# Kernel tuning notes

Measured on AMD Instinct MI355X. Metric: run time of the kernel, lower is better.

## Reference

```python
import jax, jax.numpy as jnp
import numpy as np

N_NODES = 100000
N_EDGES = 1600000
D_IN = 128
D_OUT = 128
DROP_P = 0.5


def setup_inputs() -> dict:
    key = jax.random.key(0)
    k1, k2, k3, k4, k5, k6 = jax.random.split(key, 6)
    x = jax.random.normal(k1, (N_NODES, D_IN), dtype=jnp.float32)
    # xavier_normal init for w
    std = (2.0 / (D_IN + D_OUT)) ** 0.5
    w = jax.random.normal(k2, (D_IN, D_OUT), dtype=jnp.float32) * std
    b = jax.random.normal(k3, (D_OUT,), dtype=jnp.float32) * 0.01
    edge_row = jax.random.randint(k4, (N_EDGES,), 0, N_NODES, dtype=jnp.int32)
    edge_col = jax.random.randint(k5, (N_EDGES,), 0, N_NODES, dtype=jnp.int32)
    # normalized adjacency weights (e.g. 1/sqrt(d_i d_j)); use uniform positives
    edge_val = jax.random.uniform(k6, (N_EDGES,), dtype=jnp.float32)
    # dropout mask: keep with prob (1-p), scaled by 1/(1-p)
    km = jax.random.fold_in(key, 7)
    keep = jax.random.uniform(km, (N_NODES, D_IN)) >= DROP_P
    dropout_mask = keep.astype(jnp.float32) / (1.0 - DROP_P)
    return {"x": x, "w": w, "b": b, "edge_row": edge_row,
            "edge_col": edge_col, "edge_val": edge_val,
            "dropout_mask": dropout_mask}


def reference(x, w, b, edge_row, edge_col, edge_val, dropout_mask):
    # dropout (training mode) -> dense mm -> spmm(adj, xw) -> +b -> relu
    h = (x * dropout_mask) @ w                      # [N, D_OUT]
    msgs = h[edge_col] * edge_val[:, None]          # gather src feats, scale [E, D_OUT]
    agg = jax.ops.segment_sum(msgs, edge_row, num_segments=N_NODES)  # scatter-add to dst
    return jax.nn.relu(agg + b)
```

## Files before the change

kernel.cpp:

```cpp
#include <hip/hip_runtime.h>

#define N_NODES 100000
#define N_EDGES 1600000
#define D 128
#define MAXDEG 48

#define GEMM_NB ((N_NODES + 63) / 64)
#define HIST_NB (N_EDGES / 256)
#define TOTAL_NB (GEMM_NB + HIST_NB)

typedef __attribute__((ext_vector_type(8))) short short8;
typedef __attribute__((ext_vector_type(4))) short short4v;
typedef __attribute__((ext_vector_type(4))) float floatx4;

__device__ __forceinline__ short f2bf(float f) {
    unsigned u = __float_as_uint(f);
    u += 0x7FFFu + ((u >> 16) & 1u);
    return (short)(u >> 16);
}

#define LDSK 136
__global__ __launch_bounds__(256) void gemm_hist_fill(const float* __restrict__ x,
                                                      const float* __restrict__ mask,
                                                      const float* __restrict__ w,
                                                      unsigned short* __restrict__ h,
                                                      const int* __restrict__ erow,
                                                      const int* __restrict__ ecol,
                                                      const float* __restrict__ eval,
                                                      int* __restrict__ deg,
                                                      unsigned long long* __restrict__ pairs) {
    const unsigned bid = blockIdx.x;
    if (bid % 5 != 0 || bid >= 5 * GEMM_NB) {
        const int hist_idx = (int)(bid - bid / 5 - 1 + (bid >= 5u * GEMM_NB ? 1u : 0u))
                           - (bid >= 5u * GEMM_NB ? (int)(bid - 5u * GEMM_NB) - (int)(bid - 5u * GEMM_NB) : 0);
        const int hi = (bid < 5u * GEMM_NB) ? (int)(bid - bid / 5 - 1) : (int)(bid - GEMM_NB);
        const int e = hi * 256 + threadIdx.x;
        const int r = erow[e];
        const int k = atomicAdd(&deg[r], 1);
        if (k < MAXDEG) {
            const unsigned long long v =
                (unsigned long long)(unsigned)ecol[e] |
                ((unsigned long long)(unsigned)__float_as_uint(eval[e]) << 32);
            __builtin_nontemporal_store(v, pairs + (size_t)r * MAXDEG + k);
        }
        return;
    }
    const int gb = (int)(bid / 5);

    __shared__ short w_s[128 * LDSK];
    const int t = threadIdx.x;

#pragma unroll
    for (int i = 0; i < 4; ++i) {
        const int id = t + 256 * i;
        const int n0 = (id & 31) * 4;
        const int k0 = (id >> 5) * 4;
        short tr[4][4];
#pragma unroll
        for (int r = 0; r < 4; ++r) {
            const float4 wv = *(const float4*)(w + (size_t)(k0 + r) * D + n0);
            tr[r][0] = f2bf(wv.x); tr[r][1] = f2bf(wv.y);
            tr[r][2] = f2bf(wv.z); tr[r][3] = f2bf(wv.w);
        }
#pragma unroll
        for (int c = 0; c < 4; ++c) {
            short4v v = {tr[0][c], tr[1][c], tr[2][c], tr[3][c]};
            *(short4v*)(&w_s[(n0 + c) * LDSK + k0]) = v;
        }
    }
    __syncthreads();

    const int wave = t >> 6, lane = t & 63;
    const int m = lane & 15, quad = lane >> 4;
    const int r0w = gb * 64 + wave * 16;
    int arow = r0w + m;
    if (arow >= N_NODES) arow = N_NODES - 1;
    const float* xp = x + (size_t)arow * D;
    const float* mp = mask + (size_t)arow * D;

    floatx4 acc[8];
#pragma unroll
    for (int tt = 0; tt < 8; ++tt) acc[tt] = (floatx4){0.f, 0.f, 0.f, 0.f};

#pragma unroll
    for (int kc = 0; kc < 4; ++kc) {
        const int kb = kc * 32 + quad * 8;
        const float4 xa = *(const float4*)(xp + kb);
        const float4 xb = *(const float4*)(xp + kb + 4);
        const float4 ma = *(const float4*)(mp + kb);
        const float4 mb = *(const float4*)(mp + kb + 4);
        short8 a;
        a[0] = f2bf(xa.x * ma.x); a[1] = f2bf(xa.y * ma.y);
        a[2] = f2bf(xa.z * ma.z); a[3] = f2bf(xa.w * ma.w);
        a[4] = f2bf(xb.x * mb.x); a[5] = f2bf(xb.y * mb.y);
        a[6] = f2bf(xb.z * mb.z); a[7] = f2bf(xb.w * mb.w);
#pragma unroll
        for (int tt = 0; tt < 8; ++tt) {
            const short8 bfrag = *(const short8*)(&w_s[(tt * 16 + m) * LDSK + kb]);
            acc[tt] = __builtin_amdgcn_mfma_f32_16x16x32_bf16(a, bfrag, acc[tt], 0, 0, 0);
        }
    }

    __syncthreads();
    short* ep = w_s + wave * 16 * LDSK;
#pragma unroll
    for (int tt = 0; tt < 8; ++tt) {
        const int col = tt * 16 + m;
#pragma unroll
        for (int i = 0; i < 4; ++i)
            ep[(quad * 4 + i) * LDSK + col] = f2bf(acc[tt][i]);
    }
    __syncthreads();

    const int rrow = lane >> 2;
    const int chunk = lane & 3;
    const int gr = r0w + rrow;
    if (gr < N_NODES) {
        const short* src = ep + rrow * LDSK + chunk * 32;
        unsigned short* dst = h + (size_t)gr * D + chunk * 32;
#pragma unroll
        for (int j = 0; j < 4; ++j)
            *(short8*)(dst + j * 8) = *(const short8*)(src + j * 8);
    }
}

__global__ __launch_bounds__(256) void gather_kernel(const unsigned* __restrict__ h2,
                                                     const int* __restrict__ deg,
                                                     const int2* __restrict__ pairs,
                                                     const float* __restrict__ b,
                                                     float* __restrict__ out) {
    const int row = blockIdx.x * 4 + (threadIdx.x >> 6);
    const int lane = threadIdx.x & 63;

    int dg = deg[row];
    if (dg > MAXDEG) dg = MAXDEG;
    int p = row * MAXDEG;
    const int end = p + dg;

    float accx = 0.f, accy = 0.f;
    for (; p + 7 < end; p += 8) {
        int2 pr[8];
        unsigned u[8];
#pragma unroll
        for (int j = 0; j < 8; ++j) pr[j] = pairs[p + j];
#pragma unroll
        for (int j = 0; j < 8; ++j) u[j] = h2[(size_t)pr[j].x * 64 + lane];
#pragma unroll
        for (int j = 0; j < 8; ++j) {
            const float v = __int_as_float(pr[j].y);
            accx += __uint_as_float(u[j] << 16) * v;
            accy += __uint_as_float(u[j] & 0xFFFF0000u) * v;
        }
    }
    for (; p < end; ++p) {
        const int2 p0 = pairs[p];
        const unsigned u0 = h2[(size_t)p0.x * 64 + lane];
        const float v0 = __int_as_float(p0.y);
        accx += __uint_as_float(u0 << 16) * v0;
        accy += __uint_as_float(u0 & 0xFFFF0000u) * v0;
    }

    const float2 bv = ((const float2*)b)[lane];
    float2 o;
    o.x = fmaxf(accx + bv.x, 0.f);
    o.y = fmaxf(accy + bv.y, 0.f);
    ((float2*)(out + (size_t)row * D))[lane] = o;
}

extern "C" void kernel_launch(void* const* d_in, const int* in_sizes, int n_in,
                              void* d_out, int out_size, void* d_ws, size_t ws_size,
                              hipStream_t stream) {
    const float* x    = (const float*)d_in[0];
    const float* w    = (const float*)d_in[1];
    const float* b    = (const float*)d_in[2];
    const int*   erow = (const int*)d_in[3];
    const int*   ecol = (const int*)d_in[4];
    const float* eval = (const float*)d_in[5];
    const float* mask = (const float*)d_in[6];
    float* out = (float*)d_out;

    char* base = (char*)d_ws;
    unsigned short* h = (unsigned short*)(base);
    int* deg          = (int*)(base + 25600000);
    unsigned long long* pairs = (unsigned long long*)(base + 26000000);

    hipMemsetAsync(deg, 0, N_NODES * sizeof(int), stream);

    gemm_hist_fill<<<TOTAL_NB, 256, 0, stream>>>(x, mask, w, h, erow, ecol, eval, deg, pairs);
    gather_kernel<<<N_NODES / 4, 256, 0, stream>>>((const unsigned*)h, deg,
                                                   (const int2*)pairs, b, out);
}
```

Baseline: 339.1 us.

## Split fused GEMM/histogram kernel and add nontemporal loads and stores

Separates the interleaved GEMM and edge-bucketing blocks into two kernels, hist_fill and gemm_mfma, that run back-to-back on the same stream. It also switches streaming accesses (edge arrays, x, mask, pairs, output) to nontemporal loads and stores so they pollute the cache less. This removes the block-index decoding and branch divergence of the fused kernel. In exchange it adds a launch and loses the overlap between the atomic-heavy histogram and the compute-bound GEMM.

After: 383.1 us. 13.0% more time.

```diff
diff --git a/kernel.cpp b/kernel.cpp
--- a/kernel.cpp
+++ b/kernel.cpp
@@ -6,12 +6,11 @@
 #define MAXDEG 48
 
 #define GEMM_NB ((N_NODES + 63) / 64)
-#define HIST_NB (N_EDGES / 256)
-#define TOTAL_NB (GEMM_NB + HIST_NB)
 
 typedef __attribute__((ext_vector_type(8))) short short8;
 typedef __attribute__((ext_vector_type(4))) short short4v;
 typedef __attribute__((ext_vector_type(4))) float floatx4;
+typedef __attribute__((ext_vector_type(2))) float floatx2;
 
 __device__ __forceinline__ short f2bf(float f) {
     unsigned u = __float_as_uint(f);
@@ -19,34 +18,29 @@
     return (short)(u >> 16);
 }
 
+__global__ __launch_bounds__(256) void hist_fill(const int* __restrict__ erow,
+                                                 const int* __restrict__ ecol,
+                                                 const float* __restrict__ eval,
+                                                 int* __restrict__ deg,
+                                                 unsigned long long* __restrict__ pairs) {
+    const int e = blockIdx.x * 256 + threadIdx.x;
+    const int r = __builtin_nontemporal_load(erow + e);
+    const int k = atomicAdd(&deg[r], 1);
+    const int c = __builtin_nontemporal_load(ecol + e);
+    const float v = __builtin_nontemporal_load(eval + e);
+    if (k < MAXDEG) {
+        const unsigned long long pv =
+            (unsigned long long)(unsigned)c |
+            ((unsigned long long)(unsigned)__float_as_uint(v) << 32);
+        __builtin_nontemporal_store(pv, pairs + (size_t)r * MAXDEG + k);
+    }
+}
+
 #define LDSK 136
-__global__ __launch_bounds__(256) void gemm_hist_fill(const float* __restrict__ x,
-                                                      const float* __restrict__ mask,
-                                                      const float* __restrict__ w,
-                                                      unsigned short* __restrict__ h,
-                                                      const int* __restrict__ erow,
-                                                      const int* __restrict__ ecol,
-                                                      const float* __restrict__ eval,
-                                                      int* __restrict__ deg,
-                                                      unsigned long long* __restrict__ pairs) {
-    const unsigned bid = blockIdx.x;
-    if (bid % 5 != 0 || bid >= 5 * GEMM_NB) {
-        const int hist_idx = (int)(bid - bid / 5 - 1 + (bid >= 5u * GEMM_NB ? 1u : 0u))
-                           - (bid >= 5u * GEMM_NB ? (int)(bid - 5u * GEMM_NB) - (int)(bid - 5u * GEMM_NB) : 0);
-        const int hi = (bid < 5u * GEMM_NB) ? (int)(bid - bid / 5 - 1) : (int)(bid - GEMM_NB);
-        const int e = hi * 256 + threadIdx.x;
-        const int r = erow[e];
-        const int k = atomicAdd(&deg[r], 1);
-        if (k < MAXDEG) {
-            const unsigned long long v =
-                (unsigned long long)(unsigned)ecol[e] |
-                ((unsigned long long)(unsigned)__float_as_uint(eval[e]) << 32);
-            __builtin_nontemporal_store(v, pairs + (size_t)r * MAXDEG + k);
-        }
-        return;
-    }
-    const int gb = (int)(bid / 5);
-
+__global__ __launch_bounds__(256) void gemm_mfma(const float* __restrict__ x,
+                                                 const float* __restrict__ mask,
+                                                 const float* __restrict__ w,
+                                                 unsigned short* __restrict__ h) {
     __shared__ short w_s[128 * LDSK];
     const int t = threadIdx.x;
 
@@ -72,11 +66,11 @@
 
     const int wave = t >> 6, lane = t & 63;
     const int m = lane & 15, quad = lane >> 4;
-    const int r0w = gb * 64 + wave * 16;
+    const int r0w = blockIdx.x * 64 + wave * 16;
     int arow = r0w + m;
     if (arow >= N_NODES) arow = N_NODES - 1;
-    const float* xp = x + (size_t)arow * D;
-    const float* mp = mask + (size_t)arow * D;
+    const floatx4* xp4 = (const floatx4*)(x + (size_t)arow * D);
+    const floatx4* mp4 = (const floatx4*)(mask + (size_t)arow * D);
 
     floatx4 acc[8];
 #pragma unroll
@@ -85,15 +79,15 @@
 #pragma unroll
     for (int kc = 0; kc < 4; ++kc) {
         const int kb = kc * 32 + quad * 8;
-        const float4 xa = *(const float4*)(xp + kb);
-        const float4 xb = *(const float4*)(xp + kb + 4);
-        const float4 ma = *(const float4*)(mp + kb);
-        const float4 mb = *(const float4*)(mp + kb + 4);
+        const floatx4 xa = __builtin_nontemporal_load(xp4 + kb / 4);
+        const floatx4 xb = __builtin_nontemporal_load(xp4 + kb / 4 + 1);
+        const floatx4 ma = __builtin_nontemporal_load(mp4 + kb / 4);
+        const floatx4 mb = __builtin_nontemporal_load(mp4 + kb / 4 + 1);
         short8 a;
-        a[0] = f2bf(xa.x * ma.x); a[1] = f2bf(xa.y * ma.y);
-        a[2] = f2bf(xa.z * ma.z); a[3] = f2bf(xa.w * ma.w);
-        a[4] = f2bf(xb.x * mb.x); a[5] = f2bf(xb.y * mb.y);
-        a[6] = f2bf(xb.z * mb.z); a[7] = f2bf(xb.w * mb.w);
+#pragma unroll
+        for (int j = 0; j < 4; ++j) a[j] = f2bf(xa[j] * ma[j]);
+#pragma unroll
+        for (int j = 0; j < 4; ++j) a[4 + j] = f2bf(xb[j] * mb[j]);
 #pragma unroll
         for (int tt = 0; tt < 8; ++tt) {
             const short8 bfrag = *(const short8*)(&w_s[(tt * 16 + m) * LDSK + kb]);
@@ -126,7 +120,7 @@
 
 __global__ __launch_bounds__(256) void gather_kernel(const unsigned* __restrict__ h2,
                                                      const int* __restrict__ deg,
-                                                     const int2* __restrict__ pairs,
+                                                     const unsigned long long* __restrict__ pairs,
                                                      const float* __restrict__ b,
                                                      float* __restrict__ out) {
     const int row = blockIdx.x * 4 + (threadIdx.x >> 6);
@@ -139,32 +133,32 @@
 
     float accx = 0.f, accy = 0.f;
     for (; p + 7 < end; p += 8) {
-        int2 pr[8];
+        unsigned long long pr[8];
         unsigned u[8];
 #pragma unroll
-        for (int j = 0; j < 8; ++j) pr[j] = pairs[p + j];
+        for (int j = 0; j < 8; ++j) pr[j] = __builtin_nontemporal_load(pairs + p + j);
 #pragma unroll
-        for (int j = 0; j < 8; ++j) u[j] = h2[(size_t)pr[j].x * 64 + lane];
+        for (int j = 0; j < 8; ++j) u[j] = h2[(size_t)(unsigned)(pr[j] & 0xFFFFFFFFu) * 64 + lane];
 #pragma unroll
         for (int j = 0; j < 8; ++j) {
-            const float v = __int_as_float(pr[j].y);
+            const float v = __uint_as_float((unsigned)(pr[j] >> 32));
             accx += __uint_as_float(u[j] << 16) * v;
             accy += __uint_as_float(u[j] & 0xFFFF0000u) * v;
         }
     }
     for (; p < end; ++p) {
-        const int2 p0 = pairs[p];
-        const unsigned u0 = h2[(size_t)p0.x * 64 + lane];
-        const float v0 = __int_as_float(p0.y);
+        const unsigned long long p0 = __builtin_nontemporal_load(pairs + p);
+        const unsigned u0 = h2[(size_t)(unsigned)(p0 & 0xFFFFFFFFu) * 64 + lane];
+        const float v0 = __uint_as_float((unsigned)(p0 >> 32));
         accx += __uint_as_float(u0 << 16) * v0;
         accy += __uint_as_float(u0 & 0xFFFF0000u) * v0;
     }
 
     const float2 bv = ((const float2*)b)[lane];
-    float2 o;
+    floatx2 o;
     o.x = fmaxf(accx + bv.x, 0.f);
     o.y = fmaxf(accy + bv.y, 0.f);
-    ((float2*)(out + (size_t)row * D))[lane] = o;
+    __builtin_nontemporal_store(o, (floatx2*)(out + (size_t)row * D) + lane);
 }
 
 extern "C" void kernel_launch(void* const* d_in, const int* in_sizes, int n_in,
@@ -184,9 +178,9 @@
     int* deg          = (int*)(base + 25600000);
     unsigned long long* pairs = (unsigned long long*)(base + 26000000);
 
-    hipMemsetAsync(deg, 0, N_NODES * sizeof(int), stream);
+    (void)hipMemsetAsync(deg, 0, N_NODES * sizeof(int), stream);
 
-    gemm_hist_fill<<<TOTAL_NB, 256, 0, stream>>>(x, mask, w, h, erow, ecol, eval, deg, pairs);
-    gather_kernel<<<N_NODES / 4, 256, 0, stream>>>((const unsigned*)h, deg,
-                                                   (const int2*)pairs, b, out);
+    hist_fill<<<N_EDGES / 256, 256, 0, stream>>>(erow, ecol, eval, deg, pairs);
+    gemm_mfma<<<GEMM_NB, 256, 0, stream>>>(x, mask, w, h);
+    gather_kernel<<<N_NODES / 4, 256, 0, stream>>>((const unsigned*)h, deg, pairs, b, out);
 }
```
